# Performance work log

Hardware: AMD Instinct MI355X
Metric: run time of the kernel (lower is better)

## Reference

```python
import jax, jax.numpy as jnp
import numpy as np

S, B, IN, HID, H, D, DFF, L, NC, EMB = 1024, 32, 3072, 256, 16, 16, 1024, 4, 1623, 10


def setup_inputs() -> dict:
    key = jax.random.key(0)
    ks = jax.random.split(key, 12)
    w = lambda k, shp: 0.02 * jax.random.normal(k, shp, dtype=jnp.float32)
    return {
        "x": jax.random.normal(ks[0], (S, B, IN), dtype=jnp.float32),
        "fb": jax.random.randint(ks[1], (S, B), 0, NC),
        "fc1_w": w(ks[2], (HID, IN)),
        "fc1_b": jnp.zeros((HID,), jnp.float32),
        "emb": w(ks[3], (NC, EMB)),
        "proj_w": w(ks[4], (HID, HID + EMB)),
        "proj_b": jnp.zeros((HID,), jnp.float32),
        "ln1_g": jnp.ones((L, HID), jnp.float32),
        "ln1_b": jnp.zeros((L, HID), jnp.float32),
        "slow_w": w(ks[5], (L, H * (3 * D + 1), HID)),
        "out_w": w(ks[6], (L, HID, H * D)),
        "ln2_g": jnp.ones((L, HID), jnp.float32),
        "ln2_b": jnp.zeros((L, HID), jnp.float32),
        "ff1_w": w(ks[7], (L, DFF, HID)),
        "ff1_b": jnp.zeros((L, DFF), jnp.float32),
        "ff2_w": w(ks[8], (L, HID, DFF)),
        "ff2_b": jnp.zeros((L, HID), jnp.float32),
        "outl_w": w(ks[9], (NC, HID)),
        "outl_b": jnp.zeros((NC,), jnp.float32),
    }


def _ln(x, g, b):
    m = jnp.mean(x, -1, keepdims=True)
    v = jnp.mean(jnp.square(x - m), -1, keepdims=True)
    return (x - m) * jax.lax.rsqrt(v + 1e-5) * g + b


def _delta_attn(x, g, b, sw, ow):
    # x: (S, B, HID); delta-rule fast-weight linear attention
    s, bsz, _ = x.shape
    qkvb = jnp.einsum('sbi,oi->sbo', _ln(x, g, b), sw).reshape(s, bsz, H, 3 * D + 1)
    q, k, v, beta = jnp.split(qkvb, [D, 2 * D, 3 * D], axis=-1)
    q = jax.nn.softmax(q, axis=-1)      # sum-normalized feature map
    k = jax.nn.softmax(k, axis=-1)
    beta = jax.nn.sigmoid(beta)         # (S,B,H,1)

    def step(W, inp):
        qt, kt, vt, bt = inp            # (B,H,D),(B,H,D),(B,H,D),(B,H,1)
        v_old = jnp.einsum('bhkv,bhk->bhv', W, kt)
        v_new = bt * vt + (1.0 - bt) * v_old
        W = W + jnp.einsum('bhk,bhv->bhkv', kt, v_new - v_old)
        return W, jnp.einsum('bhkv,bhk->bhv', W, qt)

    W0 = jnp.zeros((bsz, H, D, D), x.dtype)
    _, o = jax.lax.scan(step, W0, (q, k, v, beta))   # o: (S,B,H,D)
    return x + jnp.einsum('sbi,oi->sbo', o.reshape(s, bsz, H * D), ow)


def _ffn(x, g, b, w1, b1, w2, b2):
    h = jax.nn.relu(jnp.einsum('sbi,oi->sbo', _ln(x, g, b), w1) + b1)
    return x + jnp.einsum('sbi,oi->sbo', h, w2) + b2


def reference(x, fb, fc1_w, fc1_b, emb, proj_w, proj_b, ln1_g, ln1_b, slow_w,
              out_w, ln2_g, ln2_b, ff1_w, ff1_b, ff2_w, ff2_b, outl_w, outl_b):
    h = jnp.einsum('sbi,oi->sbo', x, fc1_w) + fc1_b
    h = jnp.concatenate([h, emb[fb]], axis=-1)
    h = jnp.einsum('sbi,oi->sbo', h, proj_w) + proj_b
    for l in range(L):
        h = _delta_attn(h, ln1_g[l], ln1_b[l], slow_w[l], out_w[l])
        h = _ffn(h, ln2_g[l], ln2_b[l], ff1_w[l], ff1_b[l], ff2_w[l], ff2_b[l])
    return jnp.einsum('sbi,oi->sbo', h, outl_w) + outl_b
```

## Files before the change

kernel.cpp:

```cpp
#include <hip/hip_runtime.h>
#include <hip/hip_bf16.h>

#define S_LEN  1024
#define B_SZ   32
#define IN_DIM 3072
#define HID    256
#define NHEAD  16
#define HDIM   16
#define DFF    1024
#define NLAYER 4
#define NCLS   1623
#define EMB_D  10
#define MROWS  (S_LEN * B_SZ)
#define QSTRIDE 52

using bf16   = __hip_bfloat16;
using short8 = __attribute__((ext_vector_type(8))) short;
using f32x4  = __attribute__((ext_vector_type(4))) float;

#define GLOAD16(g, l) __builtin_amdgcn_global_load_lds(                        \
    (const __attribute__((address_space(1))) void*)(g),                        \
    (__attribute__((address_space(3))) void*)(l), 16, 0, 0)

template<int FLAGS>
__global__ __launch_bounds__(256) void mgemm(
    const bf16* __restrict__ A, const bf16* __restrict__ W,
    const float* __restrict__ bias, const float* R, void* C,
    int N, int K, int Wld)
{
    __shared__ bf16 sA[2][128 * 32];
    __shared__ bf16 sB[2][128 * 32];
    const int t    = threadIdx.x;
    const int lane = t & 63;
    const int wid  = t >> 6;
    const int wr   = wid >> 1, wc = wid & 1;
    const long bm  = (long)blockIdx.x * 128;
    const int  bn  = blockIdx.y * 128;
    const int  fr  = lane & 15;
    const int  fg  = lane >> 4;
    const int  row0 = t >> 2;
    const int  kq0  = (t & 3) << 3;

    f32x4 acc[4][4];
#pragma unroll
    for (int m = 0; m < 4; ++m)
#pragma unroll
        for (int n = 0; n < 4; ++n)
#pragma unroll
            for (int r = 0; r < 4; ++r) acc[m][n][r] = 0.f;

    const int nkt = K >> 5;

    auto stage = [&](int buf, int kt) {
        const int k0 = kt << 5;
        GLOAD16(A + (bm + row0)      * (long)K   + k0 + kq0, &sA[buf][(t      ) * 8]);
        GLOAD16(A + (bm + row0 + 64) * (long)K   + k0 + kq0, &sA[buf][(t + 256) * 8]);
        GLOAD16(W + (long)(bn + row0)      * Wld + k0 + kq0, &sB[buf][(t      ) * 8]);
        GLOAD16(W + (long)(bn + row0 + 64) * Wld + k0 + kq0, &sB[buf][(t + 256) * 8]);
    };

    stage(0, 0);
    __syncthreads();
    for (int kt = 0; kt < nkt; ++kt) {
        const int cur = kt & 1;
        if (kt + 1 < nkt) stage(cur ^ 1, kt + 1);
        short8 af[4], bg[4];
#pragma unroll
        for (int m = 0; m < 4; ++m)
            af[m] = *(const short8*)&sA[cur][(wr * 64 + m * 16 + fr) * 32 + fg * 8];
#pragma unroll
        for (int n = 0; n < 4; ++n)
            bg[n] = *(const short8*)&sB[cur][(wc * 64 + n * 16 + fr) * 32 + fg * 8];
#pragma unroll
        for (int m = 0; m < 4; ++m)
#pragma unroll
            for (int n = 0; n < 4; ++n)
                acc[m][n] = __builtin_amdgcn_mfma_f32_16x16x32_bf16(
                    af[m], bg[n], acc[m][n], 0, 0, 0);
        __syncthreads();
    }

    float bs[4];
#pragma unroll
    for (int n = 0; n < 4; ++n) {
        const int c = bn + wc * 64 + n * 16 + fr;
        bs[n] = ((FLAGS & 1) && c < N) ? bias[c] : 0.f;
    }
#pragma unroll
    for (int m = 0; m < 4; ++m) {
#pragma unroll
        for (int n = 0; n < 4; ++n) {
            const int c = bn + wc * 64 + n * 16 + fr;
            if (c < N) {
#pragma unroll
                for (int r = 0; r < 4; ++r) {
                    const long rw = bm + wr * 64 + m * 16 + fg * 4 + r;
                    float v = acc[m][n][r] + bs[n];
                    if (FLAGS & 2) v = fmaxf(v, 0.f);
                    if (FLAGS & 4) v += R[rw * N + c];
                    if (FLAGS & 16) {
                        const int s = (int)(rw >> 5), b = (int)(rw & 31);
                        const int hh = c / 49, cc = c - hh * 49;
                        ((float*)C)[((long)(b * 16 + hh) * 1024 + s) * QSTRIDE + cc] = v;
                    } else if (FLAGS & 8) {
                        ((bf16*)C)[rw * N + c] = __float2bfloat16(v);
                    } else {
                        ((float*)C)[rw * N + c] = v;
                    }
                }
            }
        }
    }
}

__global__ __launch_bounds__(256) void cvt8(const float* __restrict__ s,
                                            bf16* __restrict__ d, long n8)
{
    for (long i = (long)blockIdx.x * 256 + threadIdx.x; i < n8;
         i += (long)gridDim.x * 256) {
        const float4 a = ((const float4*)s)[i * 2];
        const float4 b = ((const float4*)s)[i * 2 + 1];
        alignas(16) bf16 t[8];
        t[0] = __float2bfloat16(a.x); t[1] = __float2bfloat16(a.y);
        t[2] = __float2bfloat16(a.z); t[3] = __float2bfloat16(a.w);
        t[4] = __float2bfloat16(b.x); t[5] = __float2bfloat16(b.y);
        t[6] = __float2bfloat16(b.z); t[7] = __float2bfloat16(b.w);
        ((short8*)d)[i] = *(const short8*)t;
    }
}

__global__ __launch_bounds__(256) void cvtpad(const float* __restrict__ s,
                                              bf16* __restrict__ d,
                                              int rows, int cols, int prows, int pcols)
{
    const long tot = (long)prows * pcols;
    for (long i = (long)blockIdx.x * 256 + threadIdx.x; i < tot;
         i += (long)gridDim.x * 256) {
        const int r = (int)(i / pcols), c = (int)(i - (long)r * pcols);
        d[i] = (r < rows && c < cols) ? __float2bfloat16(s[(long)r * cols + c])
                                      : __float2bfloat16(0.f);
    }
}

__global__ __launch_bounds__(256) void ln_b(
    const float* __restrict__ x, const float* __restrict__ g,
    const float* __restrict__ b, bf16* __restrict__ y)
{
    const int wave = threadIdx.x >> 6, lane = threadIdx.x & 63;
    const long row = (long)(blockIdx.x << 2) + wave;
    const float4 v = ((const float4*)(x + row * HID))[lane];
    float s = v.x + v.y + v.z + v.w;
#pragma unroll
    for (int m = 32; m; m >>= 1) s += __shfl_xor(s, m);
    const float mean = s * (1.f / 256.f);
    const float d0 = v.x - mean, d1 = v.y - mean, d2 = v.z - mean, d3 = v.w - mean;
    float ss = d0 * d0 + d1 * d1 + d2 * d2 + d3 * d3;
#pragma unroll
    for (int m = 32; m; m >>= 1) ss += __shfl_xor(ss, m);
    const float inv = rsqrtf(ss * (1.f / 256.f) + 1e-5f);
    const float4 gg = ((const float4*)g)[lane];
    const float4 bb = ((const float4*)b)[lane];
    alignas(8) bf16 t[4];
    t[0] = __float2bfloat16(fmaf(d0 * inv, gg.x, bb.x));
    t[1] = __float2bfloat16(fmaf(d1 * inv, gg.y, bb.y));
    t[2] = __float2bfloat16(fmaf(d2 * inv, gg.z, bb.z));
    t[3] = __float2bfloat16(fmaf(d3 * inv, gg.w, bb.w));
    *(ushort4*)((unsigned short*)y + row * HID + lane * 4) = *(const ushort4*)t;
}

__global__ __launch_bounds__(64) void concat_b(
    const bf16* __restrict__ ab, const float* __restrict__ emb,
    const int* __restrict__ fb, bf16* __restrict__ hcat)
{
    const long row = blockIdx.x;
    const int lane = threadIdx.x;
    const ushort4 v = ((const ushort4*)(ab + row * HID))[lane];
    ((ushort4*)(hcat + row * 288))[lane] = v;
    if (lane < 32) {
        bf16 val = (lane < EMB_D)
            ? __float2bfloat16(emb[(long)fb[row] * EMB_D + lane])
            : __float2bfloat16(0.f);
        hcat[row * 288 + 256 + lane] = val;
    }
}

#define DOT16(dst, kr, s0, s1, s2, s3) do {                                    \
    float _pa = fmaf(kr[3],  (s0).w, fmaf(kr[2],  (s0).z, fmaf(kr[1],  (s0).y, kr[0]  * (s0).x))); \
    float _pb = fmaf(kr[7],  (s1).w, fmaf(kr[6],  (s1).z, fmaf(kr[5],  (s1).y, kr[4]  * (s1).x))); \
    float _pc = fmaf(kr[11], (s2).w, fmaf(kr[10], (s2).z, fmaf(kr[9],  (s2).y, kr[8]  * (s2).x))); \
    float _pd = fmaf(kr[15], (s3).w, fmaf(kr[14], (s3).z, fmaf(kr[13], (s3).y, kr[12] * (s3).x))); \
    dst = (_pa + _pb) + (_pc + _pd);                                           \
} while (0)

__global__ __launch_bounds__(64) void scan8(
    const float* __restrict__ qkvb, bf16* __restrict__ o)
{
    __shared__ float sbuf[2][1792];
    __shared__ float W0l[16 * 20];
    __shared__ float Gm[16 * 17];
    __shared__ float QKm[16 * 17];
    __shared__ float DVl[16 * 20];
    const int lane = threadIdx.x;
    const int i4 = lane >> 2;
    const int jq = lane & 3;
    const int chain = blockIdx.x;
    const int b = chain >> 4, hh = chain & 15;
    const float* cb = qkvb + (long)chain * S_LEN * QSTRIDE;
    bf16* po = o + (long)b * HID + hh * HDIM + jq * 4;

    for (int z = lane; z < 320; z += 64) W0l[z] = 0.f;

    auto stage = [&](int buf, int nb2) {
#pragma unroll
        for (int iss = 0; iss < 7; ++iss) {
            const float* src = cb + (long)nb2 * 1664 + iss * 256 + lane * 4;
            GLOAD16(src, &sbuf[buf][iss * 256 + lane * 4]);
        }
    };

    stage(0, 0);
    asm volatile("s_waitcnt vmcnt(0)" ::: "memory");
    for (int nb = 0; nb < 32; ++nb) {
        const int buf = nb & 1;
        asm volatile("s_waitcnt vmcnt(2)" ::: "memory");
        if (nb + 1 < 32) stage(buf ^ 1, nb + 1);

        float* sb = sbuf[buf];
        {
            float* p = sb + (lane >> 1) * 52 + ((lane & 1) << 4);
            float4 a0 = *(float4*)(p),     a1 = *(float4*)(p + 4);
            float4 a2 = *(float4*)(p + 8), a3 = *(float4*)(p + 12);
            float mx = fmaxf(fmaxf(fmaxf(a0.x, a0.y), fmaxf(a0.z, a0.w)),
                             fmaxf(fmaxf(a1.x, a1.y), fmaxf(a1.z, a1.w)));
            mx = fmaxf(mx, fmaxf(fmaxf(fmaxf(a2.x, a2.y), fmaxf(a2.z, a2.w)),
                                 fmaxf(fmaxf(a3.x, a3.y), fmaxf(a3.z, a3.w))));
            a0.x = __expf(a0.x - mx); a0.y = __expf(a0.y - mx);
            a0.z = __expf(a0.z - mx); a0.w = __expf(a0.w - mx);
            a1.x = __expf(a1.x - mx); a1.y = __expf(a1.y - mx);
            a1.z = __expf(a1.z - mx); a1.w = __expf(a1.w - mx);
            a2.x = __expf(a2.x - mx); a2.y = __expf(a2.y - mx);
            a2.z = __expf(a2.z - mx); a2.w = __expf(a2.w - mx);
            a3.x = __expf(a3.x - mx); a3.y = __expf(a3.y - mx);
            a3.z = __expf(a3.z - mx); a3.w = __expf(a3.w - mx);
            const float sum = ((a0.x + a0.y) + (a0.z + a0.w))
                            + ((a1.x + a1.y) + (a1.z + a1.w))
                            + ((a2.x + a2.y) + (a2.z + a2.w))
                            + ((a3.x + a3.y) + (a3.z + a3.w));
            const float inv = 1.f / sum;
            a0.x *= inv; a0.y *= inv; a0.z *= inv; a0.w *= inv;
            a1.x *= inv; a1.y *= inv; a1.z *= inv; a1.w *= inv;
            a2.x *= inv; a2.y *= inv; a2.z *= inv; a2.w *= inv;
            a3.x *= inv; a3.y *= inv; a3.z *= inv; a3.w *= inv;
            *(float4*)(p)      = a0; *(float4*)(p + 4)  = a1;
            *(float4*)(p + 8)  = a2; *(float4*)(p + 12) = a3;
            if (!(lane & 1)) p[48] = 1.f / (1.f + __expf(-p[48]));
        }
        asm volatile("s_waitcnt lgkmcnt(0)" ::: "memory");

#pragma unroll
        for (int t = 0; t < 2; ++t) {
            const float* rb = sb + t * 16 * 52;
            const float* myrow = rb + i4 * 52;
            float ki[16], qi[16];
            {
                const float4 kA = *(const float4*)(myrow + 16);
                const float4 kB = *(const float4*)(myrow + 20);
                const float4 kC = *(const float4*)(myrow + 24);
                const float4 kD = *(const float4*)(myrow + 28);
                ki[0]=kA.x; ki[1]=kA.y; ki[2]=kA.z; ki[3]=kA.w;
                ki[4]=kB.x; ki[5]=kB.y; ki[6]=kB.z; ki[7]=kB.w;
                ki[8]=kC.x; ki[9]=kC.y; ki[10]=kC.z; ki[11]=kC.w;
                ki[12]=kD.x; ki[13]=kD.y; ki[14]=kD.z; ki[15]=kD.w;
                const float4 qA = *(const float4*)(myrow);
                const float4 qB = *(const float4*)(myrow + 4);
                const float4 qC = *(const float4*)(myrow + 8);
                const float4 qD = *(const float4*)(myrow + 12);
                qi[0]=qA.x; qi[1]=qA.y; qi[2]=qA.z; qi[3]=qA.w;
                qi[4]=qB.x; qi[5]=qB.y; qi[6]=qB.z; qi[7]=qB.w;
                qi[8]=qC.x; qi[9]=qC.y; qi[10]=qC.z; qi[11]=qC.w;
                qi[12]=qD.x; qi[13]=qD.y; qi[14]=qD.z; qi[15]=qD.w;
            }
            const float beta = myrow[48];
#pragma unroll
            for (int m = 0; m < 4; ++m) {
                const int s = jq * 4 + m;
                const float* sr = rb + s * 52 + 16;
                const float4 s0 = *(const float4*)(sr);
                const float4 s1 = *(const float4*)(sr + 4);
                const float4 s2 = *(const float4*)(sr + 8);
                const float4 s3 = *(const float4*)(sr + 12);
                float g, qk;
                DOT16(g, ki, s0, s1, s2, s3);
                DOT16(qk, qi, s0, s1, s2, s3);
                Gm[i4 * 17 + s]  = (s < i4)  ? -beta * g : 0.f;
                QKm[i4 * 17 + s] = (s <= i4) ? qk : 0.f;
            }
            float P0=0,P1=0,P2=0,P3=0, O0=0,O1=0,O2=0,O3=0;
#pragma unroll
            for (int x = 0; x < 16; ++x) {
                const float4 w = *(const float4*)&W0l[x * 20 + jq * 4];
                P0 = fmaf(ki[x], w.x, P0); P1 = fmaf(ki[x], w.y, P1);
                P2 = fmaf(ki[x], w.z, P2); P3 = fmaf(ki[x], w.w, P3);
                O0 = fmaf(qi[x], w.x, O0); O1 = fmaf(qi[x], w.y, O1);
                O2 = fmaf(qi[x], w.z, O2); O3 = fmaf(qi[x], w.w, O3);
            }
            const float4 vv = *(const float4*)(myrow + 32 + jq * 4);
            float d0 = beta * (vv.x - P0), d1 = beta * (vv.y - P1);
            float d2 = beta * (vv.z - P2), d3 = beta * (vv.w - P3);
            asm volatile("s_waitcnt lgkmcnt(0)" ::: "memory");
#pragma unroll
            for (int s = 0; s < 15; ++s) {
                const float cf = Gm[i4 * 17 + s];
                const float e0 = __shfl(d0, s * 4 + jq);
                const float e1 = __shfl(d1, s * 4 + jq);
                const float e2 = __shfl(d2, s * 4 + jq);
                const float e3 = __shfl(d3, s * 4 + jq);
                d0 = fmaf(cf, e0, d0); d1 = fmaf(cf, e1, d1);
                d2 = fmaf(cf, e2, d2); d3 = fmaf(cf, e3, d3);
            }
            f32x4 dvv; dvv[0]=d0; dvv[1]=d1; dvv[2]=d2; dvv[3]=d3;
            *(f32x4*)&DVl[i4 * 20 + jq * 4] = dvv;
            asm volatile("s_waitcnt lgkmcnt(0)" ::: "memory");
#pragma unroll
            for (int s = 0; s < 16; ++s) {
                const float c = QKm[i4 * 17 + s];
                const float4 dvs = *(const float4*)&DVl[s * 20 + jq * 4];
                O0 = fmaf(c, dvs.x, O0); O1 = fmaf(c, dvs.y, O1);
                O2 = fmaf(c, dvs.z, O2); O3 = fmaf(c, dvs.w, O3);
            }
            {
                const int sg = nb * 32 + t * 16 + i4;
                alignas(8) bf16 tb[4];
                tb[0] = __float2bfloat16(O0); tb[1] = __float2bfloat16(O1);
                tb[2] = __float2bfloat16(O2); tb[3] = __float2bfloat16(O3);
                *(ushort4*)((unsigned short*)(po + (long)sg * (B_SZ * HID))) =
                    *(const ushort4*)tb;
            }
            float a0=0,a1=0,a2=0,a3=0;
#pragma unroll
            for (int ii = 0; ii < 16; ++ii) {
                const float kx = rb[ii * 52 + 16 + i4];
                const float4 dvs = *(const float4*)&DVl[ii * 20 + jq * 4];
                a0 = fmaf(kx, dvs.x, a0); a1 = fmaf(kx, dvs.y, a1);
                a2 = fmaf(kx, dvs.z, a2); a3 = fmaf(kx, dvs.w, a3);
            }
            {
                float4 w = *(const float4*)&W0l[i4 * 20 + jq * 4];
                w.x += a0; w.y += a1; w.z += a2; w.w += a3;
                *(float4*)&W0l[i4 * 20 + jq * 4] = w;
            }
            asm volatile("s_waitcnt lgkmcnt(0)" ::: "memory");
        }
    }
}

extern "C" void kernel_launch(void* const* d_in, const int* in_sizes, int n_in,
                              void* d_out, int out_size, void* d_ws, size_t ws_size,
                              hipStream_t stream)
{
    const float* x      = (const float*)d_in[0];
    const int*   fb     = (const int*)  d_in[1];
    const float* fc1_w  = (const float*)d_in[2];
    const float* fc1_b  = (const float*)d_in[3];
    const float* emb    = (const float*)d_in[4];
    const float* proj_w = (const float*)d_in[5];
    const float* proj_b = (const float*)d_in[6];
    const float* ln1_g  = (const float*)d_in[7];
    const float* ln1_b  = (const float*)d_in[8];
    const float* slow_w = (const float*)d_in[9];
    const float* out_w  = (const float*)d_in[10];
    const float* ln2_g  = (const float*)d_in[11];
    const float* ln2_b  = (const float*)d_in[12];
    const float* ff1_w  = (const float*)d_in[13];
    const float* ff1_b  = (const float*)d_in[14];
    const float* ff2_w  = (const float*)d_in[15];
    const float* ff2_b  = (const float*)d_in[16];
    const float* outl_w = (const float*)d_in[17];
    const float* outl_b = (const float*)d_in[18];

    char* wp = (char*)d_ws;
    float* h    = (float*)wp;                 wp += (size_t)MROWS * HID * 4;
    bf16*  abuf = (bf16*)wp;                  wp += (size_t)MROWS * HID * 2;
    bf16*  fc1b = (bf16*)wp;                  wp += (size_t)HID * IN_DIM * 2;
    bf16*  projb= (bf16*)wp;                  wp += (size_t)HID * 288 * 2;
    bf16*  slowb= (bf16*)wp;                  wp += (size_t)NLAYER * 896 * HID * 2;
    bf16*  outwb= (bf16*)wp;                  wp += (size_t)NLAYER * HID * HID * 2;
    bf16*  ff1b = (bf16*)wp;                  wp += (size_t)NLAYER * DFF * HID * 2;
    bf16*  ff2b = (bf16*)wp;                  wp += (size_t)NLAYER * HID * DFF * 2;
    bf16*  outlb= (bf16*)wp;                  wp += (size_t)1664 * HID * 2;

    bf16*  xb   = (bf16*)d_out;
    bf16*  hcat = (bf16*)d_out;
    float* qkvb = (float*)d_out;
    bf16*  hff  = (bf16*)d_out;

    const dim3 blk(256);

    cvt8<<<dim3(4096), blk, 0, stream>>>(x, xb, (long)MROWS * IN_DIM / 8);
    cvt8<<<dim3(384),  blk, 0, stream>>>(fc1_w, fc1b, (long)HID * IN_DIM / 8);
    cvtpad<<<dim3(288), blk, 0, stream>>>(proj_w, projb, HID, HID + EMB_D, HID, 288);
    for (int l = 0; l < NLAYER; ++l)
        cvtpad<<<dim3(896), blk, 0, stream>>>(slow_w + (size_t)l * 784 * HID,
                                              slowb + (size_t)l * 896 * HID,
                                              784, HID, 896, HID);
    cvt8<<<dim3(128), blk, 0, stream>>>(out_w, outwb, (long)NLAYER * HID * HID / 8);
    cvt8<<<dim3(512), blk, 0, stream>>>(ff1_w, ff1b, (long)NLAYER * DFF * HID / 8);
    cvt8<<<dim3(512), blk, 0, stream>>>(ff2_w, ff2b, (long)NLAYER * HID * DFF / 8);
    cvtpad<<<dim3(1664), blk, 0, stream>>>(outl_w, outlb, NCLS, HID, 1664, HID);

    mgemm<9><<<dim3(256, 2), blk, 0, stream>>>(xb, fc1b, fc1_b, nullptr, abuf,
                                               HID, IN_DIM, IN_DIM);
    concat_b<<<dim3(MROWS), dim3(64), 0, stream>>>(abuf, emb, fb, hcat);
    mgemm<1><<<dim3(256, 2), blk, 0, stream>>>(hcat, projb, proj_b, nullptr, h,
                                               HID, 288, 288);

    for (int l = 0; l < NLAYER; ++l) {
        ln_b<<<dim3(MROWS / 4), blk, 0, stream>>>(h, ln1_g + l * HID, ln1_b + l * HID, abuf);
        mgemm<16><<<dim3(256, 7), blk, 0, stream>>>(abuf, slowb + (size_t)l * 896 * HID,
                                                    nullptr, nullptr, qkvb, 784, HID, HID);
        scan8<<<dim3(B_SZ * NHEAD), dim3(64), 0, stream>>>(qkvb, abuf);
        mgemm<4><<<dim3(256, 2), blk, 0, stream>>>(abuf, outwb + (size_t)l * HID * HID,
                                                   nullptr, h, h, HID, HID, HID);
        ln_b<<<dim3(MROWS / 4), blk, 0, stream>>>(h, ln2_g + l * HID, ln2_b + l * HID, abuf);
        mgemm<11><<<dim3(256, 8), blk, 0, stream>>>(abuf, ff1b + (size_t)l * DFF * HID,
                                                    ff1_b + l * DFF, nullptr, hff,
                                                    DFF, HID, HID);
        mgemm<5><<<dim3(256, 2), blk, 0, stream>>>(hff, ff2b + (size_t)l * HID * DFF,
                                                   ff2_b + l * HID, h, h, HID, DFF, DFF);
    }
    cvt8<<<dim3(1024), blk, 0, stream>>>(h, abuf, (long)MROWS * HID / 8);
    mgemm<1><<<dim3(256, 13), blk, 0, stream>>>(abuf, outlb, outl_b, nullptr, d_out,
                                                NCLS, HID, HID);
}
```

Before: 1.686 ms.

## Fuse x fp32-to-bf16 conversion into fc1 GEMM, shuffle-based scan coefficients

Adds a dedicated fc1 GEMM kernel that reads fp32 activations, converts them to bf16 in registers and writes them into LDS. This removes the separate full-size conversion pass over x and its round trip through memory. The scan kernel now passes the G and QK coefficients through wave shuffles instead of shared-memory arrays, and merges the W-update accumulation into the output loop. It also folds the four per-layer slow-weight conversions into one launch. The scan change adds dead placeholder code and more shuffles, and the fused GEMM's A-path relies on register staging rather than async loads.

```diff
diff --git a/kernel.cpp b/kernel.cpp
--- a/kernel.cpp
+++ b/kernel.cpp
@@ -113,6 +113,96 @@
     }
 }
 
+__global__ __launch_bounds__(256) void fc1_k(
+    const float* __restrict__ A, const bf16* __restrict__ W,
+    const float* __restrict__ bias, bf16* __restrict__ C)
+{
+    __shared__ bf16 sA[2][128 * 32];
+    __shared__ bf16 sB[2][128 * 32];
+    const int t    = threadIdx.x;
+    const int lane = t & 63;
+    const int wid  = t >> 6;
+    const int wr   = wid >> 1, wc = wid & 1;
+    const long bm  = (long)blockIdx.x * 128;
+    const int  bn  = blockIdx.y * 128;
+    const int  fr  = lane & 15;
+    const int  fg  = lane >> 4;
+    const int  row0 = t >> 2;
+    const int  kq0  = (t & 3) << 3;
+    const int  arow = t >> 3;
+    const int  ac4  = (t & 7) << 2;
+
+    f32x4 acc[4][4];
+#pragma unroll
+    for (int m = 0; m < 4; ++m)
+#pragma unroll
+        for (int n = 0; n < 4; ++n)
+#pragma unroll
+            for (int r = 0; r < 4; ++r) acc[m][n][r] = 0.f;
+
+    auto stageB = [&](int buf, int kt) {
+        const int k0 = kt << 5;
+        GLOAD16(W + (long)(bn + row0)      * IN_DIM + k0 + kq0, &sB[buf][(t      ) * 8]);
+        GLOAD16(W + (long)(bn + row0 + 64) * IN_DIM + k0 + kq0, &sB[buf][(t + 256) * 8]);
+    };
+    float4 va[4];
+    auto loadA = [&](int kt) {
+        const int k0 = kt << 5;
+#pragma unroll
+        for (int rep = 0; rep < 4; ++rep)
+            va[rep] = *(const float4*)(A + (bm + arow + rep * 32) * (long)IN_DIM + k0 + ac4);
+    };
+    auto writeA = [&](int buf) {
+#pragma unroll
+        for (int rep = 0; rep < 4; ++rep) {
+            alignas(8) bf16 tb[4];
+            tb[0] = __float2bfloat16(va[rep].x);
+            tb[1] = __float2bfloat16(va[rep].y);
+            tb[2] = __float2bfloat16(va[rep].z);
+            tb[3] = __float2bfloat16(va[rep].w);
+            *(ushort4*)&sA[buf][(arow + rep * 32) * 32 + ac4] = *(const ushort4*)tb;
+        }
+    };
+
+    loadA(0);
+    stageB(0, 0);
+    writeA(0);
+    __syncthreads();
+    const int nkt = IN_DIM >> 5;
+    for (int kt = 0; kt < nkt; ++kt) {
+        const int cur = kt & 1;
+        if (kt + 1 < nkt) { stageB(cur ^ 1, kt + 1); loadA(kt + 1); }
+        short8 af[4], bg[4];
+#pragma unroll
+        for (int m = 0; m < 4; ++m)
+            af[m] = *(const short8*)&sA[cur][(wr * 64 + m * 16 + fr) * 32 + fg * 8];
+#pragma unroll
+        for (int n = 0; n < 4; ++n)
+            bg[n] = *(const short8*)&sB[cur][(wc * 64 + n * 16 + fr) * 32 + fg * 8];
+#pragma unroll
+        for (int m = 0; m < 4; ++m)
+#pragma unroll
+            for (int n = 0; n < 4; ++n)
+                acc[m][n] = __builtin_amdgcn_mfma_f32_16x16x32_bf16(
+                    af[m], bg[n], acc[m][n], 0, 0, 0);
+        if (kt + 1 < nkt) writeA(cur ^ 1);
+        __syncthreads();
+    }
+
+#pragma unroll
+    for (int n = 0; n < 4; ++n) {
+        const int c = bn + wc * 64 + n * 16 + fr;
+        const float bsn = bias[c];
+#pragma unroll
+        for (int m = 0; m < 4; ++m)
+#pragma unroll
+            for (int r = 0; r < 4; ++r) {
+                const long rw = bm + wr * 64 + m * 16 + fg * 4 + r;
+                C[rw * HID + c] = __float2bfloat16(acc[m][n][r] + bsn);
+            }
+    }
+}
+
 __global__ __launch_bounds__(256) void cvt8(const float* __restrict__ s,
                                             bf16* __restrict__ d, long n8)
 {
@@ -142,6 +232,21 @@
     }
 }
 
+__global__ __launch_bounds__(256) void cvtpad_slow(const float* __restrict__ s,
+                                                   bf16* __restrict__ d)
+{
+    const int l = blockIdx.y;
+    const float* src = s + (size_t)l * 784 * HID;
+    bf16* dst = d + (size_t)l * 896 * HID;
+    const long tot = (long)896 * HID;
+    for (long i = (long)blockIdx.x * 256 + threadIdx.x; i < tot;
+         i += (long)gridDim.x * 256) {
+        const int r = (int)(i / HID), c = (int)(i - (long)r * HID);
+        dst[i] = (r < 784) ? __float2bfloat16(src[(long)r * HID + c])
+                           : __float2bfloat16(0.f);
+    }
+}
+
 __global__ __launch_bounds__(256) void ln_b(
     const float* __restrict__ x, const float* __restrict__ g,
     const float* __restrict__ b, bf16* __restrict__ y)
@@ -192,13 +297,11 @@
     dst = (_pa + _pb) + (_pc + _pd);                                           \
 } while (0)
 
-__global__ __launch_bounds__(64) void scan8(
+__global__ __launch_bounds__(64) void scan9(
     const float* __restrict__ qkvb, bf16* __restrict__ o)
 {
     __shared__ float sbuf[2][1792];
     __shared__ float W0l[16 * 20];
-    __shared__ float Gm[16 * 17];
-    __shared__ float QKm[16 * 17];
     __shared__ float DVl[16 * 20];
     const int lane = threadIdx.x;
     const int i4 = lane >> 2;
@@ -281,6 +384,7 @@
                 qi[12]=qD.x; qi[13]=qD.y; qi[14]=qD.z; qi[15]=qD.w;
             }
             const float beta = myrow[48];
+            float gcf[4], qkc[4];
 #pragma unroll
             for (int m = 0; m < 4; ++m) {
                 const int s = jq * 4 + m;
@@ -292,8 +396,8 @@
                 float g, qk;
                 DOT16(g, ki, s0, s1, s2, s3);
                 DOT16(qk, qi, s0, s1, s2, s3);
-                Gm[i4 * 17 + s]  = (s < i4)  ? -beta * g : 0.f;
-                QKm[i4 * 17 + s] = (s <= i4) ? qk : 0.f;
+                gcf[m] = (s < i4)  ? -beta * g : 0.f;
+                qkc[m] = (s <= i4) ? qk : 0.f;
             }
             float P0=0,P1=0,P2=0,P3=0, O0=0,O1=0,O2=0,O3=0;
 #pragma unroll
@@ -307,10 +411,9 @@
             const float4 vv = *(const float4*)(myrow + 32 + jq * 4);
             float d0 = beta * (vv.x - P0), d1 = beta * (vv.y - P1);
             float d2 = beta * (vv.z - P2), d3 = beta * (vv.w - P3);
-            asm volatile("s_waitcnt lgkmcnt(0)" ::: "memory");
 #pragma unroll
             for (int s = 0; s < 15; ++s) {
-                const float cf = Gm[i4 * 17 + s];
+                const float cf = __shfl(gcf[s & 3], i4 * 4 + (s >> 2));
                 const float e0 = __shfl(d0, s * 4 + jq);
                 const float e1 = __shfl(d1, s * 4 + jq);
                 const float e2 = __shfl(d2, s * 4 + jq);
@@ -321,12 +424,22 @@
             f32x4 dvv; dvv[0]=d0; dvv[1]=d1; dvv[2]=d2; dvv[3]=d3;
             *(f32x4*)&DVl[i4 * 20 + jq * 4] = dvv;
             asm volatile("s_waitcnt lgkmcnt(0)" ::: "memory");
+            float a0=0,a1=0,a2=0,a3=0;
 #pragma unroll
             for (int s = 0; s < 16; ++s) {
-                const float c = QKm[i4 * 17 + s];
                 const float4 dvs = *(const float4*)&DVl[s * 20 + jq * 4];
-                O0 = fmaf(c, dvs.x, O0); O1 = fmaf(c, dvs.y, O1);
-                O2 = fmaf(c, dvs.z, O2); O3 = fmaf(c, dvs.w, O3);
+                if (s < 15 || true) {
+                    const float c = (s == 15)
+                        ? ((15 <= i4) ? qkc[3] * 0.f + __shfl(qkc[3], i4 * 4 + 3) * ((i4 == 15) ? 1.f : 0.f) + ((15 < i4) ? 0.f : 0.f) : 0.f)
+                        : 0.f;
+                    (void)c;
+                }
+                const float cqk = __shfl(qkc[s & 3], i4 * 4 + (s >> 2));
+                O0 = fmaf(cqk, dvs.x, O0); O1 = fmaf(cqk, dvs.y, O1);
+                O2 = fmaf(cqk, dvs.z, O2); O3 = fmaf(cqk, dvs.w, O3);
+                const float kx = rb[s * 52 + 16 + i4];
+                a0 = fmaf(kx, dvs.x, a0); a1 = fmaf(kx, dvs.y, a1);
+                a2 = fmaf(kx, dvs.z, a2); a3 = fmaf(kx, dvs.w, a3);
             }
             {
                 const int sg = nb * 32 + t * 16 + i4;
@@ -335,14 +448,6 @@
                 tb[2] = __float2bfloat16(O2); tb[3] = __float2bfloat16(O3);
                 *(ushort4*)((unsigned short*)(po + (long)sg * (B_SZ * HID))) =
                     *(const ushort4*)tb;
-            }
-            float a0=0,a1=0,a2=0,a3=0;
-#pragma unroll
-            for (int ii = 0; ii < 16; ++ii) {
-                const float kx = rb[ii * 52 + 16 + i4];
-                const float4 dvs = *(const float4*)&DVl[ii * 20 + jq * 4];
-                a0 = fmaf(kx, dvs.x, a0); a1 = fmaf(kx, dvs.y, a1);
-                a2 = fmaf(kx, dvs.z, a2); a3 = fmaf(kx, dvs.w, a3);
             }
             {
                 float4 w = *(const float4*)&W0l[i4 * 20 + jq * 4];
@@ -389,27 +494,21 @@
     bf16*  ff2b = (bf16*)wp;                  wp += (size_t)NLAYER * HID * DFF * 2;
     bf16*  outlb= (bf16*)wp;                  wp += (size_t)1664 * HID * 2;
 
-    bf16*  xb   = (bf16*)d_out;
     bf16*  hcat = (bf16*)d_out;
     float* qkvb = (float*)d_out;
     bf16*  hff  = (bf16*)d_out;
 
     const dim3 blk(256);
 
-    cvt8<<<dim3(4096), blk, 0, stream>>>(x, xb, (long)MROWS * IN_DIM / 8);
     cvt8<<<dim3(384),  blk, 0, stream>>>(fc1_w, fc1b, (long)HID * IN_DIM / 8);
     cvtpad<<<dim3(288), blk, 0, stream>>>(proj_w, projb, HID, HID + EMB_D, HID, 288);
-    for (int l = 0; l < NLAYER; ++l)
-        cvtpad<<<dim3(896), blk, 0, stream>>>(slow_w + (size_t)l * 784 * HID,
-                                              slowb + (size_t)l * 896 * HID,
-                                              784, HID, 896, HID);
+    cvtpad_slow<<<dim3(896, 4), blk, 0, stream>>>(slow_w, slowb);
     cvt8<<<dim3(128), blk, 0, stream>>>(out_w, outwb, (long)NLAYER * HID * HID / 8);
     cvt8<<<dim3(512), blk, 0, stream>>>(ff1_w, ff1b, (long)NLAYER * DFF * HID / 8);
     cvt8<<<dim3(512), blk, 0, stream>>>(ff2_w, ff2b, (long)NLAYER * HID * DFF / 8);
     cvtpad<<<dim3(1664), blk, 0, stream>>>(outl_w, outlb, NCLS, HID, 1664, HID);
 
-    mgemm<9><<<dim3(256, 2), blk, 0, stream>>>(xb, fc1b, fc1_b, nullptr, abuf,
-                                               HID, IN_DIM, IN_DIM);
+    fc1_k<<<dim3(256, 2), blk, 0, stream>>>(x, fc1b, fc1_b, abuf);
     concat_b<<<dim3(MROWS), dim3(64), 0, stream>>>(abuf, emb, fb, hcat);
     mgemm<1><<<dim3(256, 2), blk, 0, stream>>>(hcat, projb, proj_b, nullptr, h,
                                                HID, 288, 288);
@@ -418,7 +517,7 @@
         ln_b<<<dim3(MROWS / 4), blk, 0, stream>>>(h, ln1_g + l * HID, ln1_b + l * HID, abuf);
         mgemm<16><<<dim3(256, 7), blk, 0, stream>>>(abuf, slowb + (size_t)l * 896 * HID,
                                                     nullptr, nullptr, qkvb, 784, HID, HID);
-        scan8<<<dim3(B_SZ * NHEAD), dim3(64), 0, stream>>>(qkvb, abuf);
+        scan9<<<dim3(B_SZ * NHEAD), dim3(64), 0, stream>>>(qkvb, abuf);
         mgemm<4><<<dim3(256, 2), blk, 0, stream>>>(abuf, outwb + (size_t)l * HID * HID,
                                                    nullptr, h, h, HID, HID, HID);
         ln_b<<<dim3(MROWS / 4), blk, 0, stream>>>(h, ln2_g + l * HID, ln2_b + l * HID, abuf);
```

Measured after the change: 1.665 ms. About the same (-1.2%).
